# Kernel optimization log

Measured on AMD Instinct MI355X. Metric: run time of the kernel, lower is better.

Reference implementation:

```python
import jax, jax.numpy as jnp
import numpy as np

GROUP_SIZE = 128

def setup_inputs() -> dict:
    key = jax.random.key(0)
    k1, k2, k3 = jax.random.split(key, 3)
    B, S, K, N = 4, 128, 4096, 11008
    num_groups = K // GROUP_SIZE
    x = jax.random.normal(k1, (B, S, K), dtype=jnp.float16)
    # packed int4 weights: each byte holds two nibbles (low = even k, high = odd k)
    weight_packed = jax.random.randint(k2, (N, K // 2), 0, 256, dtype=jnp.int32)
    scales = (jax.random.uniform(k3, (N, num_groups), dtype=jnp.float16) * jnp.float16(0.1))
    return {"x": x, "weight_packed": weight_packed, "scales": scales}

def reference(x, weight_packed, scales):
    # x: (B, S, K) fp16; weight_packed: (N, K//2) int in [0,256); scales: (N, K//group_size) fp16
    N, Kp = weight_packed.shape
    K = Kp * 2
    # Unpack nibbles: even k -> low nibble, odd k -> high nibble (interleaved along K)
    low = weight_packed & 0x0F
    high = (weight_packed >> 4) & 0x0F
    w_int = jnp.stack([low, high], axis=-1).reshape(N, K).astype(jnp.float32)  # (N, K)
    # Per-group dequantization: w = scale * (q - 8)
    scale_full = jnp.repeat(scales.astype(jnp.float32), GROUP_SIZE, axis=1)    # (N, K)
    w = scale_full * (w_int - 8.0)
    # fp32 accumulation, fp16 output (matches kernel: float accum, half store)
    y = jnp.einsum('bsk,nk->bsn', x.astype(jnp.float32), w)
    return y.astype(jnp.float16)
```

## Files before the change

### kernel.cpp

```cpp
#include <hip/hip_runtime.h>


typedef __attribute__((ext_vector_type(8)))  short short8;
typedef __attribute__((ext_vector_type(16))) float f32x16;
typedef __attribute__((ext_vector_type(4)))  float f32x4;
typedef __attribute__((ext_vector_type(4)))  int   i32x4;
typedef __attribute__((ext_vector_type(2)))  int   i32x2;

#define M_DIM 512
#define N_DIM 11008
#define K_DIM 4096
#define BM 128
#define BN 64
#define BK 64
#define PAD 8
#define THREADS 256
#define NTILE_M (M_DIM / BM)
#define NTILE_N (N_DIM / BN)
#define NTILES  (NTILE_M * NTILE_N)
#define KITERS  (K_DIM / BK)
#define KB16    (K_DIM / 16)

#if defined(__has_builtin)
#  if __has_builtin(__builtin_amdgcn_cvt_pk_bf16_f32)
#    define HAVE_PK_BF16 1
#  endif
#endif
#ifndef HAVE_PK_BF16
#  define HAVE_PK_BF16 0
#endif

__device__ __forceinline__ unsigned int fbits(float f) {
    union { float f; unsigned int u; } c; c.f = f; return c.u;
}
__device__ __forceinline__ int pack2bf(float lo, float hi) {
#if HAVE_PK_BF16
    typedef __attribute__((ext_vector_type(2))) __bf16 bf16x2;
    bf16x2 p = __builtin_amdgcn_cvt_pk_bf16_f32(lo, hi);
    int r; __builtin_memcpy(&r, &p, 4);
    return r;
#else
    unsigned int ul = fbits(lo), uh = fbits(hi);
    unsigned int l = (ul + 0x7FFFu + ((ul >> 16) & 1u)) >> 16;
    unsigned int h = (uh + 0x7FFFu + ((uh >> 16) & 1u)) & 0xFFFF0000u;
    return (int)(h | l);
#endif
}

__global__ __launch_bounds__(THREADS)
void cvt_x(const float* __restrict__ x, unsigned short* __restrict__ xw)
{
    int c    = blockIdx.x * THREADS + threadIdx.x;
    int lane = c & 63;
    int kb   = (c >> 6) & (KB16 - 1);
    int mb   = c >> 14;
    int m    = mb * 32 + (lane & 31);
    int k    = kb * 16 + (lane >> 5) * 8;

    const float* src = x + (size_t)m * K_DIM + k;
    f32x4 v0 = *(const f32x4*)(src);
    f32x4 v1 = *(const f32x4*)(src + 4);
    i32x4 p;
    p[0] = pack2bf(v0[0], v0[1]);
    p[1] = pack2bf(v0[2], v0[3]);
    p[2] = pack2bf(v1[0], v1[1]);
    p[3] = pack2bf(v1[2], v1[3]);
    *(i32x4*)(xw + (size_t)c * 8) = p;
}

template<bool PRECVT>
__global__ __launch_bounds__(THREADS, 3)
void dq_gemm(const unsigned short* __restrict__ xw,
             const float* __restrict__ xf,
             const int* __restrict__ wp,
             const float* __restrict__ scales,
             float* __restrict__ out)
{
    __shared__ __align__(16) unsigned short sB[2][BN][BK + PAD];

    const int t  = threadIdx.x;
    const int bx = blockIdx.x;

    const int xcd = bx & 7;
    const int w   = bx >> 3;
    const int g_  = (w >> 1) * 8 + xcd;
    const int nb  = g_ >> 1;
    const int m_idx = ((g_ & 1) << 1) | (w & 1);

    const int m0 = m_idx * BM;
    const int n0 = nb * BN;

    const int wave = t >> 6;
    const int lane = t & 63;
    const int wm = (wave & 1) * 64;
    const int wn = (wave >> 1) * 32;
    const int lr = lane & 31;
    const int lk = (lane >> 5) * 8;

    const int tr3 = t >> 3;
    const int tc4 = (t & 7) * 4;

    i32x4 pb[2];
    float sc[2];

    auto LOADB = [&](int kk) {
        const int kb = kk * BK;
        const int gq = kb >> 7;
        #pragma unroll
        for (int i = 0; i < 2; ++i) {
            pb[i] = *(const i32x4*)(wp + (size_t)(n0 + i * 32 + tr3) * (K_DIM / 2) + (kb >> 1) + tc4);
            sc[i] = scales[(size_t)(n0 + i * 32 + tr3) * (K_DIM / 128) + gq];
        }
    };

    auto WRITEB = [&](int buf) {
        #pragma unroll
        for (int i = 0; i < 2; ++i) {
            float s = sc[i], ns8 = s * -8.0f;
            i32x4 res;
            #pragma unroll
            for (int e = 0; e < 4; ++e) {
                int b = pb[i][e];
                res[e] = pack2bf((float)(b & 15) * s + ns8,
                                 (float)((b >> 4) & 15) * s + ns8);
            }
            *(i32x4*)&sB[buf][i * 32 + tr3][tc4 * 2] = res;
        }
    };

    f32x16 acc[2] = {};

    const short8* xa8 = (const short8*)xw;
    const size_t abase = ((size_t)((m0 + wm) >> 5) * KB16) * 64 + lane;

    auto MFMA_PHASE = [&](int buf, int kb) {
        __builtin_amdgcn_s_setprio(1);
        #pragma unroll
        for (int ks = 0; ks < BK; ks += 16) {
            short8 a[2], b;
            if constexpr (PRECVT) {
                const size_t ab = abase + (size_t)((kb + ks) >> 4) * 64;
                a[0] = xa8[ab];
                a[1] = xa8[ab + (size_t)KB16 * 64];
            } else {
                #pragma unroll
                for (int i = 0; i < 2; ++i) {
                    const float* src = xf + (size_t)(m0 + wm + i * 32 + lr) * K_DIM + kb + ks + lk;
                    f32x4 v0 = *(const f32x4*)(src);
                    f32x4 v1 = *(const f32x4*)(src + 4);
                    i32x4 p;
                    p[0] = pack2bf(v0[0], v0[1]);
                    p[1] = pack2bf(v0[2], v0[3]);
                    p[2] = pack2bf(v1[0], v1[1]);
                    p[3] = pack2bf(v1[2], v1[3]);
                    __builtin_memcpy(&a[i], &p, 16);
                }
            }
            b = *(const short8*)&sB[buf][wn + lr][ks + lk];
            acc[0] = __builtin_amdgcn_mfma_f32_32x32x16_bf16(a[0], b, acc[0], 0, 0, 0);
            acc[1] = __builtin_amdgcn_mfma_f32_32x32x16_bf16(a[1], b, acc[1], 0, 0, 0);
        }
        __builtin_amdgcn_s_setprio(0);
    };

    LOADB(0);
    WRITEB(0);
    __syncthreads();

    for (int kk = 0; kk < KITERS - 1; ++kk) {
        const int cur = kk & 1;
        LOADB(kk + 1);
        MFMA_PHASE(cur, kk * BK);
        WRITEB(cur ^ 1);
        __syncthreads();
    }
    MFMA_PHASE((KITERS - 1) & 1, (KITERS - 1) * BK);

    const int rbase = (lane >> 5) * 4;
    #pragma unroll
    for (int i = 0; i < 2; ++i) {
        int mg0 = m0 + wm + i * 32 + rbase;
        int ng  = n0 + wn + lr;
        #pragma unroll
        for (int r = 0; r < 16; ++r)
            out[(size_t)(mg0 + (r & 3) + 8 * (r >> 2)) * N_DIM + ng] = acc[i][r];
    }
}

extern "C" void kernel_launch(void* const* d_in, const int* in_sizes, int n_in,
                              void* d_out, int out_size, void* d_ws, size_t ws_size,
                              hipStream_t stream) {
    (void)in_sizes; (void)n_in; (void)out_size;
    const float* x      = (const float*)d_in[0];
    const int*   wpck   = (const int*)d_in[1];
    const float* scales = (const float*)d_in[2];
    float*       out    = (float*)d_out;

    const size_t XW_BYTES = (size_t)M_DIM * K_DIM * 2;

    if (ws_size >= XW_BYTES) {
        unsigned short* xw = (unsigned short*)d_ws;
        cvt_x<<<(M_DIM * K_DIM) / (THREADS * 8), THREADS, 0, stream>>>(x, xw);
        dq_gemm<true><<<NTILES, THREADS, 0, stream>>>(xw, x, wpck, scales, out);
    } else {
        dq_gemm<false><<<NTILES, THREADS, 0, stream>>>(nullptr, x, wpck, scales, out);
    }
}
```

Baseline: 254.6 us.

## Single-buffer dequantized B tile, register-prefetch A fragments, remap blocks per XCD

```diff
diff --git a/kernel.cpp b/kernel.cpp
--- a/kernel.cpp
+++ b/kernel.cpp
@@ -13,7 +13,6 @@
 #define BM 128
 #define BN 64
 #define BK 64
-#define PAD 8
 #define THREADS 256
 #define NTILE_M (M_DIM / BM)
 #define NTILE_N (N_DIM / BN)
@@ -69,23 +68,21 @@
 }
 
 template<bool PRECVT>
-__global__ __launch_bounds__(THREADS, 3)
+__global__ __launch_bounds__(THREADS, 4)
 void dq_gemm(const unsigned short* __restrict__ xw,
              const float* __restrict__ xf,
              const int* __restrict__ wp,
              const float* __restrict__ scales,
              float* __restrict__ out)
 {
-    __shared__ __align__(16) unsigned short sB[2][BN][BK + PAD];
+    __shared__ __align__(16) unsigned short sB[BN][BK + 8];
 
     const int t  = threadIdx.x;
     const int bx = blockIdx.x;
 
-    const int xcd = bx & 7;
-    const int w   = bx >> 3;
-    const int g_  = (w >> 1) * 8 + xcd;
-    const int nb  = g_ >> 1;
-    const int m_idx = ((g_ & 1) << 1) | (w & 1);
+    const int G     = (bx & 7) * 86 + (bx >> 3);
+    const int nb    = G >> 2;
+    const int m_idx = G & 3;
 
     const int m0 = m_idx * BM;
     const int n0 = nb * BN;
@@ -95,92 +92,100 @@
     const int wm = (wave & 1) * 64;
     const int wn = (wave >> 1) * 32;
     const int lr = lane & 31;
-    const int lk = (lane >> 5) * 8;
+    const int hi = lane >> 5;
+    const int lk = hi * 8;
 
     const int tr3 = t >> 3;
-    const int tc4 = (t & 7) * 4;
-
-    i32x4 pb[2];
+    const int tu4 = (t & 7) * 4;
+
+    const int wrow = (n0 + tr3) * (K_DIM / 2) + tu4;
+    const int srow = (n0 + tr3) * (K_DIM / 128);
+
+    i32x4 pbr[2];
     float sc[2];
 
     auto LOADB = [&](int kk) {
-        const int kb = kk * BK;
-        const int gq = kb >> 7;
+        const int w0 = kk * (BK / 2);
+        pbr[0] = *(const i32x4*)(wp + wrow + w0);
+        pbr[1] = *(const i32x4*)(wp + wrow + 32 * (K_DIM / 2) + w0);
+        sc[0] = scales[srow + (kk >> 1)];
+        sc[1] = scales[srow + 32 * (K_DIM / 128) + (kk >> 1)];
+    };
+
+    auto WRITEB = [&]() {
         #pragma unroll
         for (int i = 0; i < 2; ++i) {
-            pb[i] = *(const i32x4*)(wp + (size_t)(n0 + i * 32 + tr3) * (K_DIM / 2) + (kb >> 1) + tc4);
-            sc[i] = scales[(size_t)(n0 + i * 32 + tr3) * (K_DIM / 128) + gq];
-        }
-    };
-
-    auto WRITEB = [&](int buf) {
-        #pragma unroll
-        for (int i = 0; i < 2; ++i) {
-            float s = sc[i], ns8 = s * -8.0f;
+            const float s = sc[i], ns8 = s * -8.0f;
             i32x4 res;
             #pragma unroll
             for (int e = 0; e < 4; ++e) {
-                int b = pb[i][e];
+                int b = pbr[i][e];
                 res[e] = pack2bf((float)(b & 15) * s + ns8,
                                  (float)((b >> 4) & 15) * s + ns8);
             }
-            *(i32x4*)&sB[buf][i * 32 + tr3][tc4 * 2] = res;
+            *(i32x4*)&sB[i * 32 + tr3][tu4 * 2] = res;
         }
     };
 
+    const short8* xa8 = (const short8*)xw;
+    const int mb0 = (m0 + wm) >> 5;
+    const int ab0 = (mb0 * KB16) * 64 + lane;
+    const int ab1 = ((mb0 + 1) * KB16) * 64 + lane;
+
+    auto LOADA = [&](int kk, int s4, short8 (&dst)[2]) {
+        if constexpr (PRECVT) {
+            const int kadd = (kk * 4 + s4) * 64;
+            dst[0] = xa8[ab0 + kadd];
+            dst[1] = xa8[ab1 + kadd];
+        } else {
+            #pragma unroll
+            for (int i = 0; i < 2; ++i) {
+                const float* src = xf + (size_t)(m0 + wm + i * 32 + lr) * K_DIM
+                                      + kk * BK + s4 * 16 + lk;
+                f32x4 v0 = *(const f32x4*)(src);
+                f32x4 v1 = *(const f32x4*)(src + 4);
+                i32x4 p;
+                p[0] = pack2bf(v0[0], v0[1]);
+                p[1] = pack2bf(v0[2], v0[3]);
+                p[2] = pack2bf(v1[0], v1[1]);
+                p[3] = pack2bf(v1[2], v1[3]);
+                __builtin_memcpy(&dst[i], &p, 16);
+            }
+        }
+    };
+
     f32x16 acc[2] = {};
-
-    const short8* xa8 = (const short8*)xw;
-    const size_t abase = ((size_t)((m0 + wm) >> 5) * KB16) * 64 + lane;
-
-    auto MFMA_PHASE = [&](int buf, int kb) {
-        __builtin_amdgcn_s_setprio(1);
-        #pragma unroll
-        for (int ks = 0; ks < BK; ks += 16) {
-            short8 a[2], b;
-            if constexpr (PRECVT) {
-                const size_t ab = abase + (size_t)((kb + ks) >> 4) * 64;
-                a[0] = xa8[ab];
-                a[1] = xa8[ab + (size_t)KB16 * 64];
-            } else {
-                #pragma unroll
-                for (int i = 0; i < 2; ++i) {
-                    const float* src = xf + (size_t)(m0 + wm + i * 32 + lr) * K_DIM + kb + ks + lk;
-                    f32x4 v0 = *(const f32x4*)(src);
-                    f32x4 v1 = *(const f32x4*)(src + 4);
-                    i32x4 p;
-                    p[0] = pack2bf(v0[0], v0[1]);
-                    p[1] = pack2bf(v0[2], v0[3]);
-                    p[2] = pack2bf(v1[0], v1[1]);
-                    p[3] = pack2bf(v1[2], v1[3]);
-                    __builtin_memcpy(&a[i], &p, 16);
-                }
-            }
-            b = *(const short8*)&sB[buf][wn + lr][ks + lk];
-            acc[0] = __builtin_amdgcn_mfma_f32_32x32x16_bf16(a[0], b, acc[0], 0, 0, 0);
-            acc[1] = __builtin_amdgcn_mfma_f32_32x32x16_bf16(a[1], b, acc[1], 0, 0, 0);
-        }
-        __builtin_amdgcn_s_setprio(0);
+    short8 aA[2], aB[2];
+
+    auto MFMA2 = [&](const short8 (&a)[2], int s4) {
+        const short8 b = *(const short8*)&sB[wn + lr][s4 * 16 + lk];
+        acc[0] = __builtin_amdgcn_mfma_f32_32x32x16_bf16(a[0], b, acc[0], 0, 0, 0);
+        acc[1] = __builtin_amdgcn_mfma_f32_32x32x16_bf16(a[1], b, acc[1], 0, 0, 0);
     };
 
     LOADB(0);
-    WRITEB(0);
-    __syncthreads();
-
-    for (int kk = 0; kk < KITERS - 1; ++kk) {
-        const int cur = kk & 1;
-        LOADB(kk + 1);
-        MFMA_PHASE(cur, kk * BK);
-        WRITEB(cur ^ 1);
+    LOADA(0, 0, aA);
+
+    for (int kk = 0; kk < KITERS; ++kk) {
+        WRITEB();
+        __syncthreads();
+        if (kk + 1 < KITERS)
+            LOADB(kk + 1);
+
+        LOADA(kk, 1, aB);  MFMA2(aA, 0);
+        LOADA(kk, 2, aA);  MFMA2(aB, 1);
+        LOADA(kk, 3, aB);  MFMA2(aA, 2);
+        if (kk + 1 < KITERS) LOADA(kk + 1, 0, aA);
+        MFMA2(aB, 3);
+
         __syncthreads();
     }
-    MFMA_PHASE((KITERS - 1) & 1, (KITERS - 1) * BK);
-
-    const int rbase = (lane >> 5) * 4;
+
+    const int rbase = hi * 4;
     #pragma unroll
     for (int i = 0; i < 2; ++i) {
-        int mg0 = m0 + wm + i * 32 + rbase;
-        int ng  = n0 + wn + lr;
+        const int mg0 = m0 + wm + i * 32 + rbase;
+        const int ng  = n0 + wn + lr;
         #pragma unroll
         for (int r = 0; r < 16; ++r)
             out[(size_t)(mg0 + (r & 3) + 8 * (r >> 2)) * N_DIM + ng] = acc[i][r];
```

Measured after the change: 262.9 us. +3.3%, slower.

## Repack int4 weights into MFMA lane order and drop LDS staging

Applied to the files above, without the earlier changes.

```diff
diff --git a/kernel.cpp b/kernel.cpp
--- a/kernel.cpp
+++ b/kernel.cpp
@@ -10,16 +10,15 @@
 #define M_DIM 512
 #define N_DIM 11008
 #define K_DIM 4096
-#define BM 128
-#define BN 64
-#define BK 64
-#define PAD 8
+#define BM 64
+#define BN 128
 #define THREADS 256
+#define GTHREADS 128
 #define NTILE_M (M_DIM / BM)
 #define NTILE_N (N_DIM / BN)
 #define NTILES  (NTILE_M * NTILE_N)
-#define KITERS  (K_DIM / BK)
-#define KB16    (K_DIM / 16)
+#define KC      (K_DIM / 16)
+#define NSTRIPE (N_DIM / 32)
 
 #if defined(__has_builtin)
 #  if __has_builtin(__builtin_amdgcn_cvt_pk_bf16_f32)
@@ -52,7 +51,7 @@
 {
     int c    = blockIdx.x * THREADS + threadIdx.x;
     int lane = c & 63;
-    int kb   = (c >> 6) & (KB16 - 1);
+    int kb   = (c >> 6) & (KC - 1);
     int mb   = c >> 14;
     int m    = mb * 32 + (lane & 31);
     int k    = kb * 16 + (lane >> 5) * 8;
@@ -68,122 +67,184 @@
     *(i32x4*)(xw + (size_t)c * 8) = p;
 }
 
-template<bool PRECVT>
-__global__ __launch_bounds__(THREADS, 3)
+__global__ __launch_bounds__(THREADS)
+void repack_w(const int* __restrict__ wp, unsigned int* __restrict__ wq)
+{
+    int d      = blockIdx.x * THREADS + threadIdx.x;
+    int lane   = d & 63;
+    int k16    = (d >> 6) & (KC - 1);
+    int stripe = d >> 14;
+    int lr = lane & 31, hi = lane >> 5;
+    int row = stripe * 32 + lr;
+    int j0  = k16 * 8 + hi * 4;
+
+    i32x4 v = *(const i32x4*)(wp + (size_t)row * (K_DIM / 2) + j0);
+    unsigned int d0 =  (unsigned int)(v[0] & 15)
+                    | ((unsigned int)((v[0] >> 4) & 15) << 8)
+                    | ((unsigned int)(v[1] & 15) << 16)
+                    | ((unsigned int)((v[1] >> 4) & 15) << 24);
+    unsigned int d1 =  (unsigned int)(v[2] & 15)
+                    | ((unsigned int)((v[2] >> 4) & 15) << 8)
+                    | ((unsigned int)(v[3] & 15) << 16)
+                    | ((unsigned int)((v[3] >> 4) & 15) << 24);
+    i32x2 o; o[0] = (int)d0; o[1] = (int)d1;
+    *(i32x2*)(wq + (size_t)d * 2) = o;
+}
+
+__device__ __forceinline__ short8 deq8(i32x2 q, float s, float ns8)
+{
+    unsigned int w0 = (unsigned int)q[0], w1 = (unsigned int)q[1];
+    i32x4 r;
+    r[0] = pack2bf(fmaf((float)(w0 & 0xFF), s, ns8),
+                   fmaf((float)((w0 >> 8) & 0xFF), s, ns8));
+    r[1] = pack2bf(fmaf((float)((w0 >> 16) & 0xFF), s, ns8),
+                   fmaf((float)(w0 >> 24), s, ns8));
+    r[2] = pack2bf(fmaf((float)(w1 & 0xFF), s, ns8),
+                   fmaf((float)((w1 >> 8) & 0xFF), s, ns8));
+    r[3] = pack2bf(fmaf((float)((w1 >> 16) & 0xFF), s, ns8),
+                   fmaf((float)(w1 >> 24), s, ns8));
+    short8 out; __builtin_memcpy(&out, &r, 16);
+    return out;
+}
+
+__device__ __forceinline__ short8 deq_raw(i32x4 v, float s, float ns8)
+{
+    i32x4 r;
+    #pragma unroll
+    for (int e = 0; e < 4; ++e) {
+        int b = v[e];
+        r[e] = pack2bf((float)(b & 15) * s + ns8,
+                       (float)((b >> 4) & 15) * s + ns8);
+    }
+    short8 out; __builtin_memcpy(&out, &r, 16);
+    return out;
+}
+
+template<bool PRE>
+__global__ __launch_bounds__(GTHREADS, 2)
 void dq_gemm(const unsigned short* __restrict__ xw,
              const float* __restrict__ xf,
+             const unsigned int* __restrict__ wq,
              const int* __restrict__ wp,
              const float* __restrict__ scales,
              float* __restrict__ out)
 {
-    __shared__ __align__(16) unsigned short sB[2][BN][BK + PAD];
-
     const int t  = threadIdx.x;
     const int bx = blockIdx.x;
 
-    const int xcd = bx & 7;
-    const int w   = bx >> 3;
-    const int g_  = (w >> 1) * 8 + xcd;
-    const int nb  = g_ >> 1;
-    const int m_idx = ((g_ & 1) << 1) | (w & 1);
-
+    const int G     = (bx & 7) * 86 + (bx >> 3);
+    const int nb    = G >> 3;
+    const int m_idx = G & 7;
     const int m0 = m_idx * BM;
     const int n0 = nb * BN;
 
     const int wave = t >> 6;
     const int lane = t & 63;
-    const int wm = (wave & 1) * 64;
-    const int wn = (wave >> 1) * 32;
     const int lr = lane & 31;
-    const int lk = (lane >> 5) * 8;
-
-    const int tr3 = t >> 3;
-    const int tc4 = (t & 7) * 4;
-
-    i32x4 pb[2];
-    float sc[2];
-
-    auto LOADB = [&](int kk) {
-        const int kb = kk * BK;
-        const int gq = kb >> 7;
-        #pragma unroll
-        for (int i = 0; i < 2; ++i) {
-            pb[i] = *(const i32x4*)(wp + (size_t)(n0 + i * 32 + tr3) * (K_DIM / 2) + (kb >> 1) + tc4);
-            sc[i] = scales[(size_t)(n0 + i * 32 + tr3) * (K_DIM / 128) + gq];
-        }
-    };
-
-    auto WRITEB = [&](int buf) {
-        #pragma unroll
-        for (int i = 0; i < 2; ++i) {
-            float s = sc[i], ns8 = s * -8.0f;
-            i32x4 res;
+    const int hi = lane >> 5;
+    const int wn = wave * 64;
+
+    const short8* xa = (const short8*)xw;
+    const int ab0 = ((m0 >> 5) + 0) * (KC * 64) + lane;
+    const int ab1 = ((m0 >> 5) + 1) * (KC * 64) + lane;
+    const i32x2* wb = (const i32x2*)wq;
+    const int bb0 = ((n0 >> 5) + wave * 2 + 0) * (KC * 64) + lane;
+    const int bb1 = ((n0 >> 5) + wave * 2 + 1) * (KC * 64) + lane;
+    const int srow0 = (n0 + wn + lr) * (K_DIM / 128);
+    const int srow1 = (n0 + wn + 32 + lr) * (K_DIM / 128);
+
+    f32x16 acc[2][2] = {};
+
+    if constexpr (PRE) {
+        short8 aA[2], aB[2];
+        i32x2  qA[2], qB[2];
+
+        aA[0] = xa[ab0];      aA[1] = xa[ab1];
+        qA[0] = wb[bb0];      qA[1] = wb[bb1];
+        aB[0] = xa[ab0 + 64]; aB[1] = xa[ab1 + 64];
+        qB[0] = wb[bb0 + 64]; qB[1] = wb[bb1 + 64];
+
+        float sc0 = scales[srow0], sc1 = scales[srow1];
+        float nx0 = 0.f, nx1 = 0.f;
+
+        for (int g = 0; g < 32; ++g) {
+            if (g < 31) {
+                nx0 = scales[srow0 + g + 1];
+                nx1 = scales[srow1 + g + 1];
+            }
+            const float s0 = sc0, n80 = sc0 * -8.0f;
+            const float s1 = sc1, n81 = sc1 * -8.0f;
+
             #pragma unroll
-            for (int e = 0; e < 4; ++e) {
-                int b = pb[i][e];
-                res[e] = pack2bf((float)(b & 15) * s + ns8,
-                                 (float)((b >> 4) & 15) * s + ns8);
-            }
-            *(i32x4*)&sB[buf][i * 32 + tr3][tc4 * 2] = res;
-        }
-    };
-
-    f32x16 acc[2] = {};
-
-    const short8* xa8 = (const short8*)xw;
-    const size_t abase = ((size_t)((m0 + wm) >> 5) * KB16) * 64 + lane;
-
-    auto MFMA_PHASE = [&](int buf, int kb) {
-        __builtin_amdgcn_s_setprio(1);
-        #pragma unroll
-        for (int ks = 0; ks < BK; ks += 16) {
-            short8 a[2], b;
-            if constexpr (PRECVT) {
-                const size_t ab = abase + (size_t)((kb + ks) >> 4) * 64;
-                a[0] = xa8[ab];
-                a[1] = xa8[ab + (size_t)KB16 * 64];
-            } else {
-                #pragma unroll
-                for (int i = 0; i < 2; ++i) {
-                    const float* src = xf + (size_t)(m0 + wm + i * 32 + lr) * K_DIM + kb + ks + lk;
-                    f32x4 v0 = *(const f32x4*)(src);
-                    f32x4 v1 = *(const f32x4*)(src + 4);
-                    i32x4 p;
-                    p[0] = pack2bf(v0[0], v0[1]);
-                    p[1] = pack2bf(v0[2], v0[3]);
-                    p[2] = pack2bf(v1[0], v1[1]);
-                    p[3] = pack2bf(v1[2], v1[3]);
-                    __builtin_memcpy(&a[i], &p, 16);
+            for (int u = 0; u < 4; ++u) {
+                const int s = g * 8 + u * 2;
+                {
+                    short8 b0 = deq8(qA[0], s0, n80);
+                    short8 b1 = deq8(qA[1], s1, n81);
+                    acc[0][0] = __builtin_amdgcn_mfma_f32_32x32x16_bf16(aA[0], b0, acc[0][0], 0, 0, 0);
+                    acc[1][0] = __builtin_amdgcn_mfma_f32_32x32x16_bf16(aA[1], b0, acc[1][0], 0, 0, 0);
+                    acc[0][1] = __builtin_amdgcn_mfma_f32_32x32x16_bf16(aA[0], b1, acc[0][1], 0, 0, 0);
+                    acc[1][1] = __builtin_amdgcn_mfma_f32_32x32x16_bf16(aA[1], b1, acc[1][1], 0, 0, 0);
+                    if (s + 2 < KC) {
+                        aA[0] = xa[ab0 + (s + 2) * 64]; aA[1] = xa[ab1 + (s + 2) * 64];
+                        qA[0] = wb[bb0 + (s + 2) * 64]; qA[1] = wb[bb1 + (s + 2) * 64];
+                    }
+                }
+                {
+                    short8 b0 = deq8(qB[0], s0, n80);
+                    short8 b1 = deq8(qB[1], s1, n81);
+                    acc[0][0] = __builtin_amdgcn_mfma_f32_32x32x16_bf16(aB[0], b0, acc[0][0], 0, 0, 0);
+                    acc[1][0] = __builtin_amdgcn_mfma_f32_32x32x16_bf16(aB[1], b0, acc[1][0], 0, 0, 0);
+                    acc[0][1] = __builtin_amdgcn_mfma_f32_32x32x16_bf16(aB[0], b1, acc[0][1], 0, 0, 0);
+                    acc[1][1] = __builtin_amdgcn_mfma_f32_32x32x16_bf16(aB[1], b1, acc[1][1], 0, 0, 0);
+                    if (s + 3 < KC) {
+                        aB[0] = xa[ab0 + (s + 3) * 64]; aB[1] = xa[ab1 + (s + 3) * 64];
+                        qB[0] = wb[bb0 + (s + 3) * 64]; qB[1] = wb[bb1 + (s + 3) * 64];
+                    }
                 }
             }
-            b = *(const short8*)&sB[buf][wn + lr][ks + lk];
-            acc[0] = __builtin_amdgcn_mfma_f32_32x32x16_bf16(a[0], b, acc[0], 0, 0, 0);
-            acc[1] = __builtin_amdgcn_mfma_f32_32x32x16_bf16(a[1], b, acc[1], 0, 0, 0);
+            sc0 = nx0; sc1 = nx1;
         }
-        __builtin_amdgcn_s_setprio(0);
-    };
-
-    LOADB(0);
-    WRITEB(0);
-    __syncthreads();
-
-    for (int kk = 0; kk < KITERS - 1; ++kk) {
-        const int cur = kk & 1;
-        LOADB(kk + 1);
-        MFMA_PHASE(cur, kk * BK);
-        WRITEB(cur ^ 1);
-        __syncthreads();
-    }
-    MFMA_PHASE((KITERS - 1) & 1, (KITERS - 1) * BK);
-
-    const int rbase = (lane >> 5) * 4;
+    } else {
+        for (int s = 0; s < KC; ++s) {
+            const int g = s >> 3;
+            const float s0 = scales[srow0 + g], n80 = s0 * -8.0f;
+            const float s1 = scales[srow1 + g], n81 = s1 * -8.0f;
+            short8 a[2];
+            #pragma unroll
+            for (int i = 0; i < 2; ++i) {
+                const float* src = xf + (size_t)(m0 + i * 32 + lr) * K_DIM + s * 16 + hi * 8;
+                f32x4 v0 = *(const f32x4*)(src);
+                f32x4 v1 = *(const f32x4*)(src + 4);
+                i32x4 p;
+                p[0] = pack2bf(v0[0], v0[1]);
+                p[1] = pack2bf(v0[2], v0[3]);
+                p[2] = pack2bf(v1[0], v1[1]);
+                p[3] = pack2bf(v1[2], v1[3]);
+                __builtin_memcpy(&a[i], &p, 16);
+            }
+            i32x4 v0 = *(const i32x4*)(wp + (size_t)(n0 + wn + lr) * (K_DIM / 2) + s * 8 + hi * 4);
+            i32x4 v1 = *(const i32x4*)(wp + (size_t)(n0 + wn + 32 + lr) * (K_DIM / 2) + s * 8 + hi * 4);
+            short8 b0 = deq_raw(v0, s0, n80);
+            short8 b1 = deq_raw(v1, s1, n81);
+            acc[0][0] = __builtin_amdgcn_mfma_f32_32x32x16_bf16(a[0], b0, acc[0][0], 0, 0, 0);
+            acc[1][0] = __builtin_amdgcn_mfma_f32_32x32x16_bf16(a[1], b0, acc[1][0], 0, 0, 0);
+            acc[0][1] = __builtin_amdgcn_mfma_f32_32x32x16_bf16(a[0], b1, acc[0][1], 0, 0, 0);
+            acc[1][1] = __builtin_amdgcn_mfma_f32_32x32x16_bf16(a[1], b1, acc[1][1], 0, 0, 0);
+        }
+    }
+
+    const int rbase = hi * 4;
     #pragma unroll
     for (int i = 0; i < 2; ++i) {
-        int mg0 = m0 + wm + i * 32 + rbase;
-        int ng  = n0 + wn + lr;
+        const int mg0 = m0 + i * 32 + rbase;
         #pragma unroll
-        for (int r = 0; r < 16; ++r)
-            out[(size_t)(mg0 + (r & 3) + 8 * (r >> 2)) * N_DIM + ng] = acc[i][r];
+        for (int j = 0; j < 2; ++j) {
+            const int ng = n0 + wn + j * 32 + lr;
+            #pragma unroll
+            for (int r = 0; r < 16; ++r)
+                out[(size_t)(mg0 + (r & 3) + 8 * (r >> 2)) * N_DIM + ng] = acc[i][j][r];
+        }
     }
 }
 
@@ -197,12 +258,16 @@
     float*       out    = (float*)d_out;
 
     const size_t XW_BYTES = (size_t)M_DIM * K_DIM * 2;
-
-    if (ws_size >= XW_BYTES) {
+    const size_t WQ_OFF   = XW_BYTES;
+    const size_t WQ_BYTES = (size_t)NSTRIPE * KC * 64 * 8;
+
+    if (ws_size >= WQ_OFF + WQ_BYTES) {
         unsigned short* xw = (unsigned short*)d_ws;
+        unsigned int*   wq = (unsigned int*)((char*)d_ws + WQ_OFF);
         cvt_x<<<(M_DIM * K_DIM) / (THREADS * 8), THREADS, 0, stream>>>(x, xw);
-        dq_gemm<true><<<NTILES, THREADS, 0, stream>>>(xw, x, wpck, scales, out);
+        repack_w<<<(NSTRIPE * KC * 64) / THREADS, THREADS, 0, stream>>>(wpck, wq);
+        dq_gemm<true><<<NTILES, GTHREADS, 0, stream>>>(xw, x, wq, wpck, scales, out);
     } else {
-        dq_gemm<false><<<NTILES, THREADS, 0, stream>>>(nullptr, x, wpck, scales, out);
-    }
-}
+        dq_gemm<false><<<NTILES, GTHREADS, 0, stream>>>(nullptr, x, nullptr, wpck, scales, out);
+    }
+}
```

After: 302.5 us. +18.8%, slower.
